# Optimization experiments

Hardware: AMD Instinct MI355X
Metric: run time of the kernel (lower is better)

Reference implementation:

```python
import jax, jax.numpy as jnp
import numpy as np

N = 8192
IN_F = 256
OUT_F = 128
ALPHA = 0.2  # leakyrelu slope
NEG_BIG = -9e15


def setup_inputs() -> dict:
    key = jax.random.key(0)
    k1, k2, k3, k4 = jax.random.split(key, 4)
    x = jax.random.normal(k1, (N, IN_F), dtype=jnp.float32)
    adj = (jax.random.uniform(k2, (N, N)) < 0.01).astype(jnp.float32)
    adj = jnp.maximum(adj, jnp.eye(N, dtype=jnp.float32))
    # xavier-uniform-style init scales
    W = jax.random.uniform(k3, (IN_F, OUT_F), dtype=jnp.float32,
                           minval=-1.0, maxval=1.0) * np.sqrt(6.0 / (IN_F + OUT_F))
    a = jax.random.uniform(k4, (2 * OUT_F, 1), dtype=jnp.float32,
                           minval=-1.0, maxval=1.0) * np.sqrt(6.0 / (2 * OUT_F + 1))
    return {"x": x, "adj": adj, "W": W, "a": a}


def reference(x, adj, W, a):
    # h = x @ W  -> (N, F)
    h = x @ W
    # e_ij = leakyrelu(a^T [h_i || h_j]) = leakyrelu((h @ a1)_i + (h @ a2)_j)
    # equivalent to torch's repeat/cat construction, without the N^2*2F tensor
    a1 = a[:OUT_F, 0]   # (F,)
    a2 = a[OUT_F:, 0]   # (F,)
    s1 = h @ a1         # (N,)
    s2 = h @ a2         # (N,)
    e = s1[:, None] + s2[None, :]                      # (N, N)
    e = jnp.where(e > 0, e, ALPHA * e)                 # leakyrelu
    att = jnp.where(adj > 0, e, NEG_BIG)
    att = jax.nn.softmax(att, axis=1)                  # (N, N)
    # dropout is identity in eval mode
    h_prime = att @ h                                  # (N, F)
    return jax.nn.elu(h_prime)
```

## Files before the change

kernel.cpp:

```cpp
#include <hip/hip_runtime.h>
#include <cstdint>
#include <cstddef>

#define N 8192
#define IN_F 256
#define OUT_F 128
#define ALPHA 0.2f
#define CAP 256
typedef unsigned long long ull;
typedef float f32x4 __attribute__((ext_vector_type(4)));

__device__ __forceinline__ float bf2f(unsigned short u) {
    return __uint_as_float(((unsigned)u) << 16);
}
__device__ __forceinline__ unsigned short f2bf(float f) {
    unsigned x = __float_as_uint(f);
    unsigned r = (x + 0x7FFFu + ((x >> 16) & 1u)) >> 16;
    return (unsigned short)r;
}

__global__ __launch_bounds__(256, 8) void gat_all(const float* __restrict__ adj,
                                                  const float* __restrict__ x,
                                                  const float* __restrict__ W,
                                                  const float* __restrict__ a,
                                                  unsigned short* __restrict__ hb,
                                                  float* __restrict__ s1,
                                                  float* __restrict__ s2,
                                                  int* done,
                                                  float* __restrict__ out) {
    __shared__ __align__(16) float smem[4736];
    const int tid  = threadIdx.x;
    const int wv   = tid >> 6;
    const int lane = tid & 63;
    const int bid  = blockIdx.x;

    if (bid < 512) {
        float* xsT = smem;
        float* wsh = smem + 640;
        const int R0 = bid * 16;
        const int r0 = (tid >> 5) * 2;
        const int c0 = (tid & 31) * 4;

        float acc[2][4];
#pragma unroll
        for (int r = 0; r < 2; ++r)
#pragma unroll
            for (int c = 0; c < 4; ++c) acc[r][c] = 0.f;

        for (int k0 = 0; k0 < IN_F; k0 += 32) {
            if (tid < 128) {
                const int r  = tid >> 3;
                const int k4 = tid & 7;
                const float4 v = *(const float4*)(x + (size_t)(R0 + r) * IN_F + k0 + k4 * 4);
                xsT[(k4 * 4 + 0) * 20 + r] = v.x;
                xsT[(k4 * 4 + 1) * 20 + r] = v.y;
                xsT[(k4 * 4 + 2) * 20 + r] = v.z;
                xsT[(k4 * 4 + 3) * 20 + r] = v.w;
            }
#pragma unroll
            for (int q = 0; q < 4; ++q) {
                const int f = tid + q * 256;
                *(float4*)(wsh + f * 4) = *(const float4*)(W + (size_t)k0 * OUT_F + f * 4);
            }
            __syncthreads();
#pragma unroll 8
            for (int kk = 0; kk < 32; ++kk) {
                const float4 wv4 = *(const float4*)(wsh + kk * 128 + c0);
                const float2 xv  = *(const float2*)(xsT + kk * 20 + r0);
                acc[0][0] += xv.x * wv4.x; acc[0][1] += xv.x * wv4.y; acc[0][2] += xv.x * wv4.z; acc[0][3] += xv.x * wv4.w;
                acc[1][0] += xv.y * wv4.x; acc[1][1] += xv.y * wv4.y; acc[1][2] += xv.y * wv4.z; acc[1][3] += xv.y * wv4.w;
            }
            __syncthreads();
        }

#pragma unroll
        for (int r = 0; r < 2; ++r) {
            ushort4 o4;
            o4.x = f2bf(acc[r][0]); o4.y = f2bf(acc[r][1]);
            o4.z = f2bf(acc[r][2]); o4.w = f2bf(acc[r][3]);
            *(ushort4*)(hb + (size_t)(R0 + r0 + r) * OUT_F + c0) = o4;
        }
        const float4 a1v = *(const float4*)(a + c0);
        const float4 a2v = *(const float4*)(a + OUT_F + c0);
#pragma unroll
        for (int r = 0; r < 2; ++r) {
            float p1 = acc[r][0] * a1v.x + acc[r][1] * a1v.y + acc[r][2] * a1v.z + acc[r][3] * a1v.w;
            float p2 = acc[r][0] * a2v.x + acc[r][1] * a2v.y + acc[r][2] * a2v.z + acc[r][3] * a2v.w;
#pragma unroll
            for (int off = 16; off > 0; off >>= 1) {
                p1 += __shfl_xor(p1, off);
                p2 += __shfl_xor(p2, off);
            }
            if ((tid & 31) == 0) {
                s1[R0 + r0 + r] = p1;
                s2[R0 + r0 + r] = p2;
            }
        }
        __threadfence();
        __syncthreads();
        if (tid == 0)
            __hip_atomic_fetch_add(done, 1, __ATOMIC_RELEASE, __HIP_MEMORY_SCOPE_AGENT);
    }

    int*   jlw = ((int*)smem) + wv * CAP;
    float* elw = (smem + 1024) + wv * CAP;
    const int row = bid * 4 + wv;
    const f32x4* __restrict__ arow = (const f32x4*)(adj + (size_t)row * N);
    const ull below = (1ull << lane) - 1ull;

    int tot = 0;
    f32x4 va[4], vb[4];
#pragma unroll
    for (int u = 0; u < 4; ++u) va[u] = arow[lane + u * 64];

    for (int b = 0; b < 8; ++b) {
        if (b < 7) {
#pragma unroll
            for (int u = 0; u < 4; ++u) vb[u] = arow[lane + ((b + 1) * 4 + u) * 64];
        }
#pragma unroll
        for (int u = 0; u < 4; ++u) {
            const int jb = (((b * 4 + u) * 64) + lane) * 4;
            const float av[4] = {va[u].x, va[u].y, va[u].z, va[u].w};
#pragma unroll
            for (int c = 0; c < 4; ++c) {
                const bool hit = av[c] > 0.f;
                const ull m = __ballot(hit);
                if (m) {
                    const int base = tot;
                    tot += __popcll(m);
                    if (hit) {
                        const int p = base + __popcll(m & below);
                        if (p < CAP) jlw[p] = jb + c;
                    }
                }
            }
        }
#pragma unroll
        for (int u = 0; u < 4; ++u) va[u] = vb[u];
    }
    const int n = tot < CAP ? tot : CAP;

    while (__hip_atomic_load(done, __ATOMIC_ACQUIRE, __HIP_MEMORY_SCOPE_AGENT) < 512)
        __builtin_amdgcn_s_sleep(8);

    const float si = s1[row];
    float dp = 0.f;
#pragma unroll
    for (int t = 0; t < 4; ++t) {
        const int l = lane + t * 64;
        if (l < n) {
            float e = si + s2[jlw[l]];
            e = e > 0.f ? e : ALPHA * e;
            const float w = __expf(e);
            elw[l] = w;
            dp += w;
        }
    }
#pragma unroll
    for (int off = 32; off > 0; off >>= 1) dp += __shfl_xor(dp, off);
    const float denom = dp;

    const int half = lane >> 5;
    const int col4 = (lane & 31) * 4;
    float a0 = 0.f, a1 = 0.f, a2 = 0.f, a3 = 0.f;
#pragma unroll 4
    for (int l = half; l < n; l += 2) {
        const float wgt = elw[l];
        const int j = jlw[l];
        const ushort4 hv = *(const ushort4*)(hb + (size_t)j * OUT_F + col4);
        a0 += wgt * bf2f(hv.x);
        a1 += wgt * bf2f(hv.y);
        a2 += wgt * bf2f(hv.z);
        a3 += wgt * bf2f(hv.w);
    }
    a0 += __shfl_xor(a0, 32);
    a1 += __shfl_xor(a1, 32);
    a2 += __shfl_xor(a2, 32);
    a3 += __shfl_xor(a3, 32);

    if (half == 0) {
        const float r = 1.f / denom;
        float v0 = a0 * r, v1 = a1 * r, v2 = a2 * r, v3 = a3 * r;
        float4 o;
        o.x = v0 > 0.f ? v0 : (__expf(v0) - 1.f);
        o.y = v1 > 0.f ? v1 : (__expf(v1) - 1.f);
        o.z = v2 > 0.f ? v2 : (__expf(v2) - 1.f);
        o.w = v3 > 0.f ? v3 : (__expf(v3) - 1.f);
        *(float4*)(out + (size_t)row * OUT_F + col4) = o;
    }
}

__global__ __launch_bounds__(256) void gemm_xw(const float* __restrict__ x,
                                               const float* __restrict__ W,
                                               const float* __restrict__ a,
                                               unsigned short* __restrict__ hb,
                                               float* __restrict__ s1,
                                               float* __restrict__ s2) {
    __shared__ __align__(16) float xsT[64 * 20];
    __shared__ __align__(16) float ws[64 * 128];
    const int tid = threadIdx.x;
    const int R0  = blockIdx.x * 16;
    const int r0  = (tid >> 5) * 2;
    const int c0  = (tid & 31) * 4;

    float acc[2][4];
#pragma unroll
    for (int r = 0; r < 2; ++r)
#pragma unroll
        for (int c = 0; c < 4; ++c) acc[r][c] = 0.f;

    for (int k0 = 0; k0 < IN_F; k0 += 64) {
        {
            const int r  = tid >> 4;
            const int k4 = tid & 15;
            const float4 v = *(const float4*)(x + (size_t)(R0 + r) * IN_F + k0 + k4 * 4);
            xsT[(k4 * 4 + 0) * 20 + r] = v.x;
            xsT[(k4 * 4 + 1) * 20 + r] = v.y;
            xsT[(k4 * 4 + 2) * 20 + r] = v.z;
            xsT[(k4 * 4 + 3) * 20 + r] = v.w;
        }
#pragma unroll
        for (int q = 0; q < 8; ++q) {
            const int f = tid + q * 256;
            *(float4*)(ws + f * 4) = *(const float4*)(W + (size_t)k0 * OUT_F + f * 4);
        }
        __syncthreads();
#pragma unroll 8
        for (int kk = 0; kk < 64; ++kk) {
            const float4 wv = *(const float4*)(ws + kk * 128 + c0);
            const float2 xv = *(const float2*)(xsT + kk * 20 + r0);
            acc[0][0] += xv.x * wv.x; acc[0][1] += xv.x * wv.y; acc[0][2] += xv.x * wv.z; acc[0][3] += xv.x * wv.w;
            acc[1][0] += xv.y * wv.x; acc[1][1] += xv.y * wv.y; acc[1][2] += xv.y * wv.z; acc[1][3] += xv.y * wv.w;
        }
        __syncthreads();
    }
#pragma unroll
    for (int r = 0; r < 2; ++r) {
        ushort4 o4;
        o4.x = f2bf(acc[r][0]); o4.y = f2bf(acc[r][1]);
        o4.z = f2bf(acc[r][2]); o4.w = f2bf(acc[r][3]);
        *(ushort4*)(hb + (size_t)(R0 + r0 + r) * OUT_F + c0) = o4;
    }
    const float4 a1v = *(const float4*)(a + c0);
    const float4 a2v = *(const float4*)(a + OUT_F + c0);
#pragma unroll
    for (int r = 0; r < 2; ++r) {
        float p1 = acc[r][0] * a1v.x + acc[r][1] * a1v.y + acc[r][2] * a1v.z + acc[r][3] * a1v.w;
        float p2 = acc[r][0] * a2v.x + acc[r][1] * a2v.y + acc[r][2] * a2v.z + acc[r][3] * a2v.w;
#pragma unroll
        for (int off = 16; off > 0; off >>= 1) {
            p1 += __shfl_xor(p1, off);
            p2 += __shfl_xor(p2, off);
        }
        if ((tid & 31) == 0) {
            s1[R0 + r0 + r] = p1;
            s2[R0 + r0 + r] = p2;
        }
    }
}

__global__ __launch_bounds__(256, 8) void gat_fused(const float* __restrict__ adj,
                                                    const unsigned short* __restrict__ hb,
                                                    const float* __restrict__ s1,
                                                    const float* __restrict__ s2,
                                                    float* __restrict__ out) {
    const int tid  = threadIdx.x;
    const int wv   = tid >> 6;
    const int lane = tid & 63;
    const int row  = blockIdx.x * 4 + wv;

    __shared__ int   jl[4][CAP];
    __shared__ float el[4][CAP];

    const f32x4* __restrict__ arow = (const f32x4*)(adj + (size_t)row * N);
    const ull below = (1ull << lane) - 1ull;

    int tot = 0;
    f32x4 va[4], vb[4];
#pragma unroll
    for (int u = 0; u < 4; ++u) va[u] = arow[lane + u * 64];

    for (int b = 0; b < 8; ++b) {
        if (b < 7) {
#pragma unroll
            for (int u = 0; u < 4; ++u) vb[u] = arow[lane + ((b + 1) * 4 + u) * 64];
        }
#pragma unroll
        for (int u = 0; u < 4; ++u) {
            const int jb = (((b * 4 + u) * 64) + lane) * 4;
            const float av[4] = {va[u].x, va[u].y, va[u].z, va[u].w};
#pragma unroll
            for (int c = 0; c < 4; ++c) {
                const bool hit = av[c] > 0.f;
                const ull m = __ballot(hit);
                if (m) {
                    const int base = tot;
                    tot += __popcll(m);
                    if (hit) {
                        const int p = base + __popcll(m & below);
                        if (p < CAP) jl[wv][p] = jb + c;
                    }
                }
            }
        }
#pragma unroll
        for (int u = 0; u < 4; ++u) va[u] = vb[u];
    }
    const int n = tot < CAP ? tot : CAP;

    const float si = s1[row];
    float dp = 0.f;
#pragma unroll
    for (int t = 0; t < 4; ++t) {
        const int l = lane + t * 64;
        if (l < n) {
            float e = si + s2[jl[wv][l]];
            e = e > 0.f ? e : ALPHA * e;
            const float w = __expf(e);
            el[wv][l] = w;
            dp += w;
        }
    }
#pragma unroll
    for (int off = 32; off > 0; off >>= 1) dp += __shfl_xor(dp, off);
    const float denom = dp;

    const int half = lane >> 5;
    const int col4 = (lane & 31) * 4;
    float a0 = 0.f, a1 = 0.f, a2 = 0.f, a3 = 0.f;
#pragma unroll 4
    for (int l = half; l < n; l += 2) {
        const float wgt = el[wv][l];
        const int j = jl[wv][l];
        const ushort4 hv = *(const ushort4*)(hb + (size_t)j * OUT_F + col4);
        a0 += wgt * bf2f(hv.x);
        a1 += wgt * bf2f(hv.y);
        a2 += wgt * bf2f(hv.z);
        a3 += wgt * bf2f(hv.w);
    }
    a0 += __shfl_xor(a0, 32);
    a1 += __shfl_xor(a1, 32);
    a2 += __shfl_xor(a2, 32);
    a3 += __shfl_xor(a3, 32);

    if (half == 0) {
        const float r = 1.f / denom;
        float v0 = a0 * r, v1 = a1 * r, v2 = a2 * r, v3 = a3 * r;
        float4 o;
        o.x = v0 > 0.f ? v0 : (__expf(v0) - 1.f);
        o.y = v1 > 0.f ? v1 : (__expf(v1) - 1.f);
        o.z = v2 > 0.f ? v2 : (__expf(v2) - 1.f);
        o.w = v3 > 0.f ? v3 : (__expf(v3) - 1.f);
        *(float4*)(out + (size_t)row * OUT_F + col4) = o;
    }
}

extern "C" void kernel_launch(void* const* d_in, const int* in_sizes, int n_in,
                              void* d_out, int out_size, void* d_ws, size_t ws_size,
                              hipStream_t stream) {
    const float* x   = (const float*)d_in[0];
    const float* adj = (const float*)d_in[1];
    const float* W   = (const float*)d_in[2];
    const float* a   = (const float*)d_in[3];
    float* out = (float*)d_out;

    char* wsb = (char*)d_ws;
    unsigned short* hb = (unsigned short*)wsb;
    float* s1 = (float*)(wsb + 2 * 1024 * 1024);
    float* s2 = s1 + N;
    int* done = (int*)(wsb + 2 * 1024 * 1024 + 64 * 1024);

    int nb = 0;
    (void)hipOccupancyMaxActiveBlocksPerMultiprocessor(&nb, gat_all, 256, 0);
    if (nb >= 8) {
        hipMemsetAsync(done, 0, sizeof(int), stream);
        void* args[] = {(void*)&adj, (void*)&x, (void*)&W, (void*)&a,
                        (void*)&hb, (void*)&s1, (void*)&s2, (void*)&done, (void*)&out};
        hipLaunchCooperativeKernel((const void*)gat_all, dim3(2048), dim3(256),
                                   args, 0, stream);
    } else {
        gemm_xw<<<N / 16, 256, 0, stream>>>(x, W, a, hb, s1, s2);
        gat_fused<<<2048, 256, 0, stream>>>(adj, hb, s1, s2, out);
    }
}
```

Before: 70.65 us.

## Overlap neighbor aggregation with adjacency scan once projection is ready

The fused GAT kernel now polls the global done counter between adjacency-scan chunks and, once the projection stage has finished, starts accumulating softmax weights and bf16 h rows for neighbors already found, while the rest of the row is still being scanned. Every lane now computes the exp weight redundantly and handles two output columns across the full wave, replacing the two-half split, the shared-memory weight array and the cross-lane reductions. This aims to hide the wait for the projection and the gather latency behind the adjacency streaming. In exchange each lane does redundant exp and s2 loads per neighbor, and the atomic poll inside the scan loop adds overhead.

```diff
diff --git a/kernel.cpp b/kernel.cpp
--- a/kernel.cpp
+++ b/kernel.cpp
@@ -18,6 +18,7 @@
     unsigned r = (x + 0x7FFFu + ((x >> 16) & 1u)) >> 16;
     return (unsigned short)r;
 }
+__device__ __forceinline__ float lrelu(float e) { return e > 0.f ? e : ALPHA * e; }
 
 __global__ __launch_bounds__(256, 8) void gat_all(const float* __restrict__ adj,
                                                   const float* __restrict__ x,
@@ -102,13 +103,17 @@
             __hip_atomic_fetch_add(done, 1, __ATOMIC_RELEASE, __HIP_MEMORY_SCOPE_AGENT);
     }
 
-    int*   jlw = ((int*)smem) + wv * CAP;
-    float* elw = (smem + 1024) + wv * CAP;
+    int* jlw = ((int*)smem) + wv * CAP;
     const int row = bid * 4 + wv;
     const f32x4* __restrict__ arow = (const f32x4*)(adj + (size_t)row * N);
+    const unsigned* __restrict__ hb32 = (const unsigned*)hb;
     const ull below = (1ull << lane) - 1ull;
 
-    int tot = 0;
+    bool ready = false;
+    float si = 0.f;
+    int tot = 0, proc = 0;
+    float acc0 = 0.f, acc1 = 0.f, dp = 0.f;
+
     f32x4 va[4], vb[4];
 #pragma unroll
     for (int u = 0; u < 4; ++u) va[u] = arow[lane + u * 64];
@@ -136,59 +141,92 @@
                 }
             }
         }
+        if (!ready &&
+            __hip_atomic_load(done, __ATOMIC_ACQUIRE, __HIP_MEMORY_SCOPE_AGENT) >= 512) {
+            ready = true;
+            si = s1[row];
+        }
+        if (ready) {
+            const int te = tot < CAP ? tot : CAP;
+            while (proc + 4 <= te) {
+                const int j0 = jlw[proc + 0], j1 = jlw[proc + 1];
+                const int j2 = jlw[proc + 2], j3 = jlw[proc + 3];
+                const float e0 = si + s2[j0], e1 = si + s2[j1];
+                const float e2 = si + s2[j2], e3 = si + s2[j3];
+                const unsigned g0 = hb32[(size_t)j0 * 64 + lane];
+                const unsigned g1 = hb32[(size_t)j1 * 64 + lane];
+                const unsigned g2 = hb32[(size_t)j2 * 64 + lane];
+                const unsigned g3 = hb32[(size_t)j3 * 64 + lane];
+                const float w0 = __expf(lrelu(e0));
+                const float w1 = __expf(lrelu(e1));
+                const float w2 = __expf(lrelu(e2));
+                const float w3 = __expf(lrelu(e3));
+                acc0 += w0 * bf2f((unsigned short)(g0 & 0xFFFFu))
+                      + w1 * bf2f((unsigned short)(g1 & 0xFFFFu))
+                      + w2 * bf2f((unsigned short)(g2 & 0xFFFFu))
+                      + w3 * bf2f((unsigned short)(g3 & 0xFFFFu));
+                acc1 += w0 * bf2f((unsigned short)(g0 >> 16))
+                      + w1 * bf2f((unsigned short)(g1 >> 16))
+                      + w2 * bf2f((unsigned short)(g2 >> 16))
+                      + w3 * bf2f((unsigned short)(g3 >> 16));
+                dp += (w0 + w1) + (w2 + w3);
+                proc += 4;
+            }
+        }
 #pragma unroll
         for (int u = 0; u < 4; ++u) va[u] = vb[u];
     }
-    const int n = tot < CAP ? tot : CAP;
-
-    while (__hip_atomic_load(done, __ATOMIC_ACQUIRE, __HIP_MEMORY_SCOPE_AGENT) < 512)
-        __builtin_amdgcn_s_sleep(8);
-
-    const float si = s1[row];
-    float dp = 0.f;
-#pragma unroll
-    for (int t = 0; t < 4; ++t) {
-        const int l = lane + t * 64;
-        if (l < n) {
-            float e = si + s2[jlw[l]];
-            e = e > 0.f ? e : ALPHA * e;
-            const float w = __expf(e);
-            elw[l] = w;
+
+    while (!ready) {
+        if (__hip_atomic_load(done, __ATOMIC_ACQUIRE, __HIP_MEMORY_SCOPE_AGENT) >= 512) {
+            ready = true;
+            si = s1[row];
+        } else {
+            __builtin_amdgcn_s_sleep(2);
+        }
+    }
+    {
+        const int te = tot < CAP ? tot : CAP;
+        while (proc + 4 <= te) {
+            const int j0 = jlw[proc + 0], j1 = jlw[proc + 1];
+            const int j2 = jlw[proc + 2], j3 = jlw[proc + 3];
+            const float e0 = si + s2[j0], e1 = si + s2[j1];
+            const float e2 = si + s2[j2], e3 = si + s2[j3];
+            const unsigned g0 = hb32[(size_t)j0 * 64 + lane];
+            const unsigned g1 = hb32[(size_t)j1 * 64 + lane];
+            const unsigned g2 = hb32[(size_t)j2 * 64 + lane];
+            const unsigned g3 = hb32[(size_t)j3 * 64 + lane];
+            const float w0 = __expf(lrelu(e0));
+            const float w1 = __expf(lrelu(e1));
+            const float w2 = __expf(lrelu(e2));
+            const float w3 = __expf(lrelu(e3));
+            acc0 += w0 * bf2f((unsigned short)(g0 & 0xFFFFu))
+                  + w1 * bf2f((unsigned short)(g1 & 0xFFFFu))
+                  + w2 * bf2f((unsigned short)(g2 & 0xFFFFu))
+                  + w3 * bf2f((unsigned short)(g3 & 0xFFFFu));
+            acc1 += w0 * bf2f((unsigned short)(g0 >> 16))
+                  + w1 * bf2f((unsigned short)(g1 >> 16))
+                  + w2 * bf2f((unsigned short)(g2 >> 16))
+                  + w3 * bf2f((unsigned short)(g3 >> 16));
+            dp += (w0 + w1) + (w2 + w3);
+            proc += 4;
+        }
+        while (proc < te) {
+            const int j = jlw[proc++];
+            const float w = __expf(lrelu(si + s2[j]));
+            const unsigned g = hb32[(size_t)j * 64 + lane];
+            acc0 += w * bf2f((unsigned short)(g & 0xFFFFu));
+            acc1 += w * bf2f((unsigned short)(g >> 16));
             dp += w;
         }
     }
-#pragma unroll
-    for (int off = 32; off > 0; off >>= 1) dp += __shfl_xor(dp, off);
-    const float denom = dp;
-
-    const int half = lane >> 5;
-    const int col4 = (lane & 31) * 4;
-    float a0 = 0.f, a1 = 0.f, a2 = 0.f, a3 = 0.f;
-#pragma unroll 4
-    for (int l = half; l < n; l += 2) {
-        const float wgt = elw[l];
-        const int j = jlw[l];
-        const ushort4 hv = *(const ushort4*)(hb + (size_t)j * OUT_F + col4);
-        a0 += wgt * bf2f(hv.x);
-        a1 += wgt * bf2f(hv.y);
-        a2 += wgt * bf2f(hv.z);
-        a3 += wgt * bf2f(hv.w);
-    }
-    a0 += __shfl_xor(a0, 32);
-    a1 += __shfl_xor(a1, 32);
-    a2 += __shfl_xor(a2, 32);
-    a3 += __shfl_xor(a3, 32);
-
-    if (half == 0) {
-        const float r = 1.f / denom;
-        float v0 = a0 * r, v1 = a1 * r, v2 = a2 * r, v3 = a3 * r;
-        float4 o;
-        o.x = v0 > 0.f ? v0 : (__expf(v0) - 1.f);
-        o.y = v1 > 0.f ? v1 : (__expf(v1) - 1.f);
-        o.z = v2 > 0.f ? v2 : (__expf(v2) - 1.f);
-        o.w = v3 > 0.f ? v3 : (__expf(v3) - 1.f);
-        *(float4*)(out + (size_t)row * OUT_F + col4) = o;
-    }
+
+    const float r = 1.f / dp;
+    float v0 = acc0 * r, v1 = acc1 * r;
+    float2 o;
+    o.x = v0 > 0.f ? v0 : (__expf(v0) - 1.f);
+    o.y = v1 > 0.f ? v1 : (__expf(v1) - 1.f);
+    *(float2*)(out + (size_t)row * OUT_F + 2 * lane) = o;
 }
 
 __global__ __launch_bounds__(256) void gemm_xw(const float* __restrict__ x,
@@ -315,9 +353,7 @@
     for (int t = 0; t < 4; ++t) {
         const int l = lane + t * 64;
         if (l < n) {
-            float e = si + s2[jl[wv][l]];
-            e = e > 0.f ? e : ALPHA * e;
-            const float w = __expf(e);
+            const float w = __expf(lrelu(si + s2[jl[wv][l]]));
             el[wv][l] = w;
             dp += w;
         }
```

New measurement: 70.85 us. No clear change (+0.3%).
